# Kernel optimization log

Hardware: AMD Instinct MI355X
Metric: run time of the kernel (lower is better)

## Reference

```python
import jax, jax.numpy as jnp
import numpy as np

HIDDEN = 1024

def setup_inputs() -> dict:
    key = jax.random.key(0)
    k0, k1, k2, k3 = jax.random.split(key, 4)
    inputs = jax.random.normal(k0, (4, 2048, HIDDEN), dtype=jnp.float32)
    s = 1.0 / np.sqrt(HIDDEN)
    Wq = jax.random.normal(k1, (HIDDEN, HIDDEN), dtype=jnp.float32) * s
    Wk = jax.random.normal(k2, (HIDDEN, HIDDEN), dtype=jnp.float32) * s
    Wv = jax.random.normal(k3, (HIDDEN, HIDDEN), dtype=jnp.float32) * s
    return {"inputs": inputs, "Wq": Wq, "Wk": Wk, "Wv": Wv}

def reference(inputs, Wq, Wk, Wv):
    # nn.Linear with weight W applies x @ W.T; store Wq etc. as the torch weight.
    Q = jnp.einsum('bsd,ed->bse', inputs, Wq)  # [B,S,D]
    K = jnp.einsum('bsd,ed->bse', inputs, Wk)
    V = jnp.einsum('bsd,ed->bse', inputs, Wv)
    alpha = jnp.einsum('bqd,bkd->bqk', Q, K)   # no 1/sqrt(d) scaling, per source
    alpha = jax.nn.softmax(alpha, axis=2)
    return jnp.einsum('bqk,bkd->bqd', alpha, V)
```

## Files before the change

kernel.cpp:

```cpp
#include <hip/hip_runtime.h>
#include <math.h>


typedef unsigned short u16;
typedef signed char s8;
typedef __attribute__((ext_vector_type(8))) short bf16x8;
typedef __attribute__((ext_vector_type(4))) float f32x4;
typedef __attribute__((ext_vector_type(4))) int i32x4;

__device__ __forceinline__ u16 f2bf(float x) {
  unsigned u = __float_as_uint(x);
  unsigned r = (u + 0x7fffu + ((u >> 16) & 1u)) >> 16;
  return (u16)r;
}
__device__ __forceinline__ float bf2f(u16 h) {
  return __uint_as_float((unsigned)h << 16);
}
__device__ __forceinline__ int clamp127(int q) {
  return q < -127 ? -127 : (q > 127 ? 127 : q);
}

__device__ __forceinline__ void gload_lds16(const void* g, void* l) {
  __builtin_amdgcn_global_load_lds(
      (const __attribute__((address_space(1))) unsigned int*)(g),
      (__attribute__((address_space(3))) unsigned int*)(l), 16, 0, 0);
}

template <int N>
__device__ __forceinline__ void wait_vmcnt() {
  if constexpr (N == 0) asm volatile("s_waitcnt vmcnt(0)" ::: "memory");
  else if constexpr (N == 3) asm volatile("s_waitcnt vmcnt(3)" ::: "memory");
  else if constexpr (N == 4) asm volatile("s_waitcnt vmcnt(4)" ::: "memory");
  else if constexpr (N == 6) asm volatile("s_waitcnt vmcnt(6)" ::: "memory");
}

template <bool LO>
__global__ __launch_bounds__(256) void split_f32_kernel(
    const float* __restrict__ in, u16* __restrict__ hi, u16* __restrict__ lo,
    long long n) {
  long long i = ((long long)blockIdx.x * 256 + threadIdx.x) * 4;
  const long long step = (long long)gridDim.x * 256 * 4;
  for (; i < n; i += step) {
    float4 x = *(const float4*)(in + i);
    float xs[4] = {x.x, x.y, x.z, x.w};
    u16 hv[4], lv[4];
#pragma unroll
    for (int j = 0; j < 4; j++) {
      hv[j] = f2bf(xs[j]);
      if (LO) lv[j] = f2bf(xs[j] - bf2f(hv[j]));
    }
    ushort4 h;
    h.x = hv[0]; h.y = hv[1]; h.z = hv[2]; h.w = hv[3];
    *(ushort4*)(hi + i) = h;
    if (LO) {
      ushort4 l;
      l.x = lv[0]; l.y = lv[1]; l.z = lv[2]; l.w = lv[3];
      *(ushort4*)(lo + i) = l;
    }
  }
}

__global__ __launch_bounds__(256) void quantW3_kernel(
    const float* __restrict__ Wq, const float* __restrict__ Wk,
    const float* __restrict__ Wv, u16* __restrict__ Wch,
    u16* __restrict__ Wcl, u16* __restrict__ Wvh, long long n) {
  const int z = blockIdx.z;
  const float* src = (z == 0) ? Wq : ((z == 1) ? Wk : Wv);
  u16* hi = (z == 0) ? Wch : ((z == 1) ? (Wch + n) : Wvh);
  u16* lo = (z == 0) ? Wcl : ((z == 1) ? (Wcl + n) : nullptr);
  long long i = ((long long)blockIdx.x * 256 + threadIdx.x) * 4;
  const long long step = (long long)gridDim.x * 256 * 4;
  for (; i < n; i += step) {
    float4 x = *(const float4*)(src + i);
    float xs[4] = {x.x, x.y, x.z, x.w};
    u16 hv[4], lv[4];
#pragma unroll
    for (int j = 0; j < 4; j++) {
      hv[j] = f2bf(xs[j]);
      lv[j] = f2bf(xs[j] - bf2f(hv[j]));
    }
    ushort4 h;
    h.x = hv[0]; h.y = hv[1]; h.z = hv[2]; h.w = hv[3];
    *(ushort4*)(hi + i) = h;
    if (z < 2) {
      ushort4 l;
      l.x = lv[0]; l.y = lv[1]; l.z = lv[2]; l.w = lv[3];
      *(ushort4*)(lo + i) = l;
    }
  }
}

__global__ __launch_bounds__(512, 2) void gemmf(
    const u16* __restrict__ Xh, const u16* __restrict__ Xl,
    const u16* __restrict__ Wh, const u16* __restrict__ Wl,
    s8* __restrict__ Ca, s8* __restrict__ Cb) {
  constexpr int PL = 8192;
  __shared__ u16 lds[2 * 4 * PL];

  const int tid = threadIdx.x;
  const int ln = tid & 63;
  const int wid = tid >> 6;
  const int wm = wid >> 2;
  const int wn = wid & 3;
  const int m0 = blockIdx.y * 256;
  const int n0 = blockIdx.x * 256;

  f32x4 acc[8][4];
  const f32x4 zero = {0.f, 0.f, 0.f, 0.f};
#pragma unroll
  for (int i = 0; i < 8; i++)
#pragma unroll
    for (int j = 0; j < 4; j++) acc[i][j] = zero;

  auto stage = [&](int t) {
    u16* slot = lds + (t & 1) * 4 * PL;
    const int k0 = t << 5;
#pragma unroll
    for (int l = 0; l < 2; ++l) {
      const int c = tid + l * 512;
      const int row = ((c >> 6) << 4) + (c & 15);
      const int kk = ((c >> 4) & 3) * 8;
      gload_lds16(Xh + (size_t)(m0 + row) * 1024 + k0 + kk, slot + c * 8);
      gload_lds16(Xl + (size_t)(m0 + row) * 1024 + k0 + kk,
                  slot + PL + c * 8);
      gload_lds16(Wh + (size_t)(n0 + row) * 1024 + k0 + kk,
                  slot + 2 * PL + c * 8);
      gload_lds16(Wl + (size_t)(n0 + row) * 1024 + k0 + kk,
                  slot + 3 * PL + c * 8);
    }
  };

  stage(0);
  wait_vmcnt<0>();
  __builtin_amdgcn_s_barrier();
  __builtin_amdgcn_sched_barrier(0);

  for (int t = 0; t < 32; ++t) {
    if (t + 1 < 32) stage(t + 1);
    const u16* Ah = lds + (t & 1) * 4 * PL;
    const u16* Al = Ah + PL;
    const u16* Bh = Ah + 2 * PL;
    const u16* Bl = Ah + 3 * PL;
    const int fo = ln * 8;
    bf16x8 bh[4], bl[4];
#pragma unroll
    for (int j = 0; j < 4; ++j) {
      bh[j] = *(const bf16x8*)(Bh + (wn * 4 + j) * 512 + fo);
      bl[j] = *(const bf16x8*)(Bl + (wn * 4 + j) * 512 + fo);
    }
    __builtin_amdgcn_s_setprio(1);
#pragma unroll
    for (int mh = 0; mh < 2; ++mh) {
      bf16x8 ah[4], al[4];
#pragma unroll
      for (int i = 0; i < 4; ++i) {
        ah[i] = *(const bf16x8*)(Ah + (wm * 8 + mh * 4 + i) * 512 + fo);
        al[i] = *(const bf16x8*)(Al + (wm * 8 + mh * 4 + i) * 512 + fo);
      }
#pragma unroll
      for (int i = 0; i < 4; ++i)
#pragma unroll
        for (int j = 0; j < 4; ++j) {
          f32x4 v = acc[mh * 4 + i][j];
          v = __builtin_amdgcn_mfma_f32_16x16x32_bf16(ah[i], bh[j], v, 0, 0, 0);
          v = __builtin_amdgcn_mfma_f32_16x16x32_bf16(ah[i], bl[j], v, 0, 0, 0);
          v = __builtin_amdgcn_mfma_f32_16x16x32_bf16(al[i], bh[j], v, 0, 0, 0);
          acc[mh * 4 + i][j] = v;
        }
    }
    __builtin_amdgcn_s_setprio(0);
    if (t + 1 < 32) {
      wait_vmcnt<0>();
      __builtin_amdgcn_s_barrier();
      __builtin_amdgcn_sched_barrier(0);
    }
  }

  const int orow = (ln >> 4) * 4;
  const int ocol = ln & 15;
#pragma unroll
  for (int mi = 0; mi < 8; ++mi)
#pragma unroll
    for (int ni = 0; ni < 4; ++ni) {
      const int rbase = m0 + wm * 128 + mi * 16 + orow;
      const int cc = n0 + wn * 64 + ni * 16 + ocol;
#pragma unroll
      for (int i = 0; i < 4; ++i) {
        const float v = acc[mi][ni][i];
        const long long off = (long long)(rbase + i) * 2048 + cc;
        const int qa = clamp127(__float2int_rn(v * 16.f));
        const int qb = clamp127(__float2int_rn((v - qa * 0.0625f) * 2048.f));
        Ca[off] = (s8)qa;
        Cb[off] = (s8)qb;
      }
    }
}

__global__ __launch_bounds__(512, 2) void g2(
    const s8* __restrict__ Aa, const s8* __restrict__ Ab,
    const s8* __restrict__ Ba, const s8* __restrict__ Bb,
    u16* __restrict__ Ch, u16* __restrict__ Cl,
    int K, int lda, int ldb, int ldc,
    long long sA, long long sB, long long sC,
    float scaleA, float scaleC) {
  constexpr int APL = 128 * 64;
  constexpr int BPL = 256 * 64;
  constexpr int SLOT = 2 * APL + 2 * BPL;
  __shared__ s8 lds[3 * SLOT];

  const int tid = threadIdx.x;
  const int ln = tid & 63;
  const int wid = tid >> 6;
  const int wm = wid >> 2;
  const int wn = wid & 3;
  const int m0 = blockIdx.y * 128;
  const int n0 = blockIdx.x * 256;
  const int z = blockIdx.z;
  const long long za = (long long)z * sA;
  const long long zb = (long long)z * sB;

  const int NT = K >> 6;

  i32x4 accA[4][4], accC[4][4];
  const i32x4 izero = {0, 0, 0, 0};
#pragma unroll
  for (int i = 0; i < 4; i++)
#pragma unroll
    for (int j = 0; j < 4; j++) { accA[i][j] = izero; accC[i][j] = izero; }

  auto stage = [&](int t) {
    s8* slot = lds + (t % 3) * SLOT;
    const int k0 = t << 6;
    const s8* pAa = Aa + za + (size_t)m0 * lda + k0;
    const s8* pAb = Ab + za + (size_t)m0 * lda + k0;
    const s8* pBa = Ba + zb + (size_t)n0 * ldb + k0;
    const s8* pBb = Bb + zb + (size_t)n0 * ldb + k0;
    {
      const int c = tid;
      const int row = ((c >> 6) << 4) + (c & 15);
      const int kk = ((c >> 4) & 3) * 16;
      gload_lds16(pAa + (size_t)row * lda + kk, slot + c * 16);
      gload_lds16(pAb + (size_t)row * lda + kk, slot + APL + c * 16);
    }
#pragma unroll
    for (int l = 0; l < 2; ++l) {
      const int c = tid + l * 512;
      const int row = ((c >> 6) << 4) + (c & 15);
      const int kk = ((c >> 4) & 3) * 16;
      gload_lds16(pBa + (size_t)row * ldb + kk, slot + 2 * APL + c * 16);
      gload_lds16(pBb + (size_t)row * ldb + kk,
                  slot + 2 * APL + BPL + c * 16);
    }
  };

  stage(0);
  stage(1);
  wait_vmcnt<6>();
  __builtin_amdgcn_s_barrier();
  __builtin_amdgcn_sched_barrier(0);

  for (int t = 0; t < NT; ++t) {
    if (t + 2 < NT) stage(t + 2);
    const s8* Sa = lds + (t % 3) * SLOT;
    const s8* Sb = Sa + APL;
    const s8* Sba = Sa + 2 * APL;
    const s8* Sbb = Sba + BPL;
    const int fo = (ln >> 4) * 256 + (ln & 15) * 16;
    i32x4 aa[4], ab[4], ba[4], bb[4];
#pragma unroll
    for (int j = 0; j < 4; ++j) {
      ba[j] = *(const i32x4*)(Sba + (wn * 4 + j) * 1024 + fo);
      bb[j] = *(const i32x4*)(Sbb + (wn * 4 + j) * 1024 + fo);
    }
#pragma unroll
    for (int i = 0; i < 4; ++i) {
      aa[i] = *(const i32x4*)(Sa + (wm * 4 + i) * 1024 + fo);
      ab[i] = *(const i32x4*)(Sb + (wm * 4 + i) * 1024 + fo);
    }
    __builtin_amdgcn_s_setprio(1);
#pragma unroll
    for (int i = 0; i < 4; ++i)
#pragma unroll
      for (int j = 0; j < 4; ++j) {
        accA[i][j] = __builtin_amdgcn_mfma_i32_16x16x64_i8(
            aa[i], ba[j], accA[i][j], 0, 0, 0);
        accC[i][j] = __builtin_amdgcn_mfma_i32_16x16x64_i8(
            aa[i], bb[j], accC[i][j], 0, 0, 0);
        accC[i][j] = __builtin_amdgcn_mfma_i32_16x16x64_i8(
            ab[i], ba[j], accC[i][j], 0, 0, 0);
      }
    __builtin_amdgcn_s_setprio(0);
    if (t + 1 < NT) {
      if (t + 2 < NT) wait_vmcnt<6>();
      else            wait_vmcnt<0>();
      __builtin_amdgcn_s_barrier();
      __builtin_amdgcn_sched_barrier(0);
    }
  }

  const int orow = (ln >> 4) * 4;
  const int ocol = ln & 15;
#pragma unroll
  for (int mi = 0; mi < 4; ++mi)
#pragma unroll
    for (int ni = 0; ni < 4; ++ni) {
      const int rbase = m0 + wm * 64 + mi * 16 + orow;
      const int cc = n0 + wn * 64 + ni * 16 + ocol;
#pragma unroll
      for (int i = 0; i < 4; ++i) {
        const float v = (float)accA[mi][ni][i] * scaleA +
                        (float)accC[mi][ni][i] * scaleC;
        const long long off =
            (long long)(rbase + i) * ldc + cc + (long long)z * sC;
        const u16 h = f2bf(v);
        Ch[off] = h;
        Cl[off] = f2bf(v - bf2f(h));
      }
    }
}

template <int STORE>
__global__ __launch_bounds__(512, 2) void gemmc64(
    const u16* __restrict__ A0, const u16* __restrict__ B0,
    float* __restrict__ Cf, u16* __restrict__ Ch,
    int K, int lda, int ldb, int ldc,
    long long sA, long long sB, long long sC) {
  constexpr int ASZ = 128 * 64;
  constexpr int BSZ = 256 * 64;
  constexpr int SLOT = ASZ + BSZ;
  __shared__ u16 lds[3 * SLOT];

  const int tid = threadIdx.x;
  const int ln = tid & 63;
  const int wid = tid >> 6;
  const int wm = wid >> 2;
  const int wn = wid & 3;
  const int m0 = blockIdx.y * 128;
  const int n0 = blockIdx.x * 256;
  const int z = blockIdx.z;
  const long long za = (long long)z * sA;
  const long long zb = (long long)z * sB;

  const int NT = K >> 6;

  f32x4 acc[4][4];
  const f32x4 zero = {0.f, 0.f, 0.f, 0.f};
#pragma unroll
  for (int i = 0; i < 4; i++)
#pragma unroll
    for (int j = 0; j < 4; j++) acc[i][j] = zero;

  auto stage = [&](int t) {
    u16* slot = lds + (t % 3) * SLOT;
    const int k0 = t << 6;
    const u16* Ab = A0 + za + (size_t)m0 * lda + k0;
    const u16* Bb = B0 + zb + (size_t)n0 * ldb + k0;
#pragma unroll
    for (int l = 0; l < 2; ++l) {
      const int c = tid + l * 512;
      const int row = c >> 3;
      const int jg = (c & 7) ^ (row & 7);
      gload_lds16(Ab + (size_t)row * lda + jg * 8, slot + c * 8);
    }
#pragma unroll
    for (int l = 0; l < 4; ++l) {
      const int c = tid + l * 512;
      const int row = c >> 3;
      const int jg = (c & 7) ^ (row & 7);
      gload_lds16(Bb + (size_t)row * ldb + jg * 8, slot + ASZ + c * 8);
    }
  };

  stage(0);
  stage(1);
  wait_vmcnt<6>();
  __builtin_amdgcn_s_barrier();
  __builtin_amdgcn_sched_barrier(0);

  const int r15 = ln & 15;
  const int jk = ln >> 4;
  const int sw0 = ((jk ^ (r15 & 7)) * 8);
  const int sw1 = (((4 + jk) ^ (r15 & 7)) * 8);

  for (int t = 0; t < NT; ++t) {
    if (t + 2 < NT) stage(t + 2);
    const u16* Abuf = lds + (t % 3) * SLOT;
    const u16* Bbuf = Abuf + ASZ;
    bf16x8 a0[4], a1[4], b0[4], b1[4];
#pragma unroll
    for (int j = 0; j < 4; ++j) {
      const int rb = ((wn * 4 + j) * 16 + r15) * 64;
      b0[j] = *(const bf16x8*)(Bbuf + rb + sw0);
      b1[j] = *(const bf16x8*)(Bbuf + rb + sw1);
    }
#pragma unroll
    for (int i = 0; i < 4; ++i) {
      const int ra = ((wm * 4 + i) * 16 + r15) * 64;
      a0[i] = *(const bf16x8*)(Abuf + ra + sw0);
      a1[i] = *(const bf16x8*)(Abuf + ra + sw1);
    }
    __builtin_amdgcn_s_setprio(1);
#pragma unroll
    for (int i = 0; i < 4; ++i)
#pragma unroll
      for (int j = 0; j < 4; ++j) {
        acc[i][j] = __builtin_amdgcn_mfma_f32_16x16x32_bf16(
            a0[i], b0[j], acc[i][j], 0, 0, 0);
        acc[i][j] = __builtin_amdgcn_mfma_f32_16x16x32_bf16(
            a1[i], b1[j], acc[i][j], 0, 0, 0);
      }
    __builtin_amdgcn_s_setprio(0);
    if (t + 1 < NT) {
      if (t + 2 < NT) wait_vmcnt<6>();
      else            wait_vmcnt<0>();
      __builtin_amdgcn_s_barrier();
      __builtin_amdgcn_sched_barrier(0);
    }
  }

  const int orow = (ln >> 4) * 4;
  const int ocol = ln & 15;
#pragma unroll
  for (int mi = 0; mi < 4; ++mi)
#pragma unroll
    for (int ni = 0; ni < 4; ++ni) {
      const int rbase = m0 + wm * 64 + mi * 16 + orow;
      const int cc = n0 + wn * 64 + ni * 16 + ocol;
#pragma unroll
      for (int i = 0; i < 4; ++i) {
        const float v = acc[mi][ni][i];
        const long long off =
            (long long)(rbase + i) * ldc + cc + (long long)z * sC;
        if (STORE == 0) Cf[off] = v;
        else            Ch[off] = f2bf(v);
      }
    }
}

template <int NSEG, int STORE, int M_REP>
__global__ __launch_bounds__(512, 2) void gemmc(
    const u16* __restrict__ A0, const u16* __restrict__ A1,
    const u16* __restrict__ A2, const u16* __restrict__ B0,
    const u16* __restrict__ B1, const u16* __restrict__ B2,
    float* __restrict__ Cf, u16* __restrict__ Ch, u16* __restrict__ Cl,
    int Kseg, int lda, int ldb, int ldc,
    long long sA, long long sB, long long sC) {
  constexpr int BM = 32 * M_REP;
  constexpr int ASZ = BM * 32;
  constexpr int BSZ = 8192;
  constexpr int SLOT = ASZ + BSZ;
  constexpr int LA = M_REP / 4;
  constexpr int L = LA + 2;
  __shared__ u16 lds[3 * SLOT];

  const int tid = threadIdx.x;
  const int ln = tid & 63;
  const int wid = tid >> 6;
  const int wm = wid >> 2;
  const int wn = wid & 3;
  const int m0 = blockIdx.y * BM;
  const int n0 = blockIdx.x * 256;
  const int z = blockIdx.z;
  const long long za = (long long)z * sA;
  const long long zb = (long long)z * sB;

  const int NT = NSEG * (Kseg >> 5);

  f32x4 acc[M_REP][4];
  const f32x4 zero = {0.f, 0.f, 0.f, 0.f};
#pragma unroll
  for (int i = 0; i < M_REP; i++)
#pragma unroll
    for (int j = 0; j < 4; j++) acc[i][j] = zero;

  auto baseA = [&](int t) -> const u16* {
    int kk = t << 5;
    const u16* p = A0;
    if (NSEG >= 2 && kk >= Kseg) { kk -= Kseg; p = A1; }
    if (NSEG >= 3 && kk >= Kseg) { kk -= Kseg; p = A2; }
    return p + za + (size_t)m0 * lda + kk;
  };
  auto baseB = [&](int t) -> const u16* {
    int kk = t << 5;
    const u16* p = B0;
    if (NSEG >= 2 && kk >= Kseg) { kk -= Kseg; p = B1; }
    if (NSEG >= 3 && kk >= Kseg) { kk -= Kseg; p = B2; }
    return p + zb + (size_t)n0 * ldb + kk;
  };
  auto stage = [&](int t) {
    u16* slot = lds + (t % 3) * SLOT;
    const u16* Ab = baseA(t);
    const u16* Bb = baseB(t);
#pragma unroll
    for (int l = 0; l < LA; ++l) {
      const int c = tid + l * 512;
      const int row = ((c >> 6) << 4) + (c & 15);
      const int kk = ((c >> 4) & 3) * 8;
      gload_lds16(Ab + (size_t)row * lda + kk, slot + c * 8);
    }
#pragma unroll
    for (int l = 0; l < 2; ++l) {
      const int c = tid + l * 512;
      const int row = ((c >> 6) << 4) + (c & 15);
      const int kk = ((c >> 4) & 3) * 8;
      gload_lds16(Bb + (size_t)row * ldb + kk, slot + ASZ + c * 8);
    }
  };

  stage(0);
  stage(1);
  wait_vmcnt<L>();
  __builtin_amdgcn_s_barrier();
  __builtin_amdgcn_sched_barrier(0);

  for (int t = 0; t < NT; ++t) {
    if (t + 2 < NT) stage(t + 2);
    const u16* Abuf = lds + (t % 3) * SLOT;
    const u16* Bbuf = Abuf + ASZ;
    const int fo = ln * 8;
    bf16x8 a[M_REP], b[4];
#pragma unroll
    for (int j = 0; j < 4; ++j)
      b[j] = *(const bf16x8*)(Bbuf + (wn * 4 + j) * 512 + fo);
#pragma unroll
    for (int i = 0; i < M_REP; ++i)
      a[i] = *(const bf16x8*)(Abuf + (wm * M_REP + i) * 512 + fo);
    __builtin_amdgcn_s_setprio(1);
#pragma unroll
    for (int i = 0; i < M_REP; ++i)
#pragma unroll
      for (int j = 0; j < 4; ++j)
        acc[i][j] = __builtin_amdgcn_mfma_f32_16x16x32_bf16(
            a[i], b[j], acc[i][j], 0, 0, 0);
    __builtin_amdgcn_s_setprio(0);
    if (t + 1 < NT) {
      if (t + 2 < NT) wait_vmcnt<L>();
      else            wait_vmcnt<0>();
      __builtin_amdgcn_s_barrier();
      __builtin_amdgcn_sched_barrier(0);
    }
  }

  const int orow = (ln >> 4) * 4;
  const int ocol = ln & 15;
#pragma unroll
  for (int mi = 0; mi < M_REP; ++mi)
#pragma unroll
    for (int ni = 0; ni < 4; ++ni) {
      const int rbase = m0 + wm * (M_REP * 16) + mi * 16 + orow;
      const int cc = n0 + wn * 64 + ni * 16 + ocol;
#pragma unroll
      for (int i = 0; i < 4; ++i) {
        const float v = acc[mi][ni][i];
        const long long off =
            (long long)(rbase + i) * ldc + cc + (long long)z * sC;
        if (STORE == 0) {
          Cf[off] = v;
        } else if (STORE == 1) {
          const u16 h = f2bf(v);
          Ch[off] = h;
          Cl[off] = f2bf(v - bf2f(h));
        } else {
          Ch[off] = f2bf(v);
        }
      }
    }
}

__device__ __forceinline__ float blk_max(float v, float* red) {
  const int wv = threadIdx.x >> 6, lnn = threadIdx.x & 63;
#pragma unroll
  for (int off = 32; off; off >>= 1) v = fmaxf(v, __shfl_xor(v, off));
  if (lnn == 0) red[wv] = v;
  __syncthreads();
  return fmaxf(fmaxf(red[0], red[1]), fmaxf(red[2], red[3]));
}
__device__ __forceinline__ float blk_sum(float v, float* red) {
  const int wv = threadIdx.x >> 6, lnn = threadIdx.x & 63;
#pragma unroll
  for (int off = 32; off; off >>= 1) v += __shfl_xor(v, off);
  if (lnn == 0) red[wv] = v;
  __syncthreads();
  return red[0] + red[1] + red[2] + red[3];
}

__global__ __launch_bounds__(256) void softmax_inplace(float* __restrict__ L) {
  float* p = L + (size_t)blockIdx.x * 2048;
  const int t = threadIdx.x;
  __shared__ float redm[4];
  __shared__ float reds[4];
  float4 x0 = *(const float4*)(p + t * 4);
  float4 x1 = *(const float4*)(p + 1024 + t * 4);
  float m = fmaxf(fmaxf(fmaxf(x0.x, x0.y), fmaxf(x0.z, x0.w)),
                  fmaxf(fmaxf(x1.x, x1.y), fmaxf(x1.z, x1.w)));
  m = blk_max(m, redm);
  float e[8];
  e[0] = __expf(x0.x - m); e[1] = __expf(x0.y - m);
  e[2] = __expf(x0.z - m); e[3] = __expf(x0.w - m);
  e[4] = __expf(x1.x - m); e[5] = __expf(x1.y - m);
  e[6] = __expf(x1.z - m); e[7] = __expf(x1.w - m);
  float s = e[0] + e[1] + e[2] + e[3] + e[4] + e[5] + e[6] + e[7];
  s = blk_sum(s, reds);
  const float inv = 1.f / s;
  u16* q = (u16*)p;
  ushort4 o0, o1;
  o0.x = f2bf(e[0] * inv); o0.y = f2bf(e[1] * inv);
  o0.z = f2bf(e[2] * inv); o0.w = f2bf(e[3] * inv);
  o1.x = f2bf(e[4] * inv); o1.y = f2bf(e[5] * inv);
  o1.z = f2bf(e[6] * inv); o1.w = f2bf(e[7] * inv);
  *(ushort4*)(q + t * 4) = o0;
  *(ushort4*)(q + 1024 + t * 4) = o1;
}

__global__ __launch_bounds__(256) void softmax_split(
    u16* __restrict__ Lh, const u16* __restrict__ Ll) {
  u16* ph = Lh + (size_t)blockIdx.x * 2048;
  const u16* pl = Ll + (size_t)blockIdx.x * 2048;
  const int t = threadIdx.x;
  __shared__ float redm[4];
  __shared__ float reds[4];
  ushort4 h0 = *(const ushort4*)(ph + t * 4);
  ushort4 h1 = *(const ushort4*)(ph + 1024 + t * 4);
  ushort4 l0 = *(const ushort4*)(pl + t * 4);
  ushort4 l1 = *(const ushort4*)(pl + 1024 + t * 4);
  float x[8];
  x[0] = bf2f(h0.x) + bf2f(l0.x); x[1] = bf2f(h0.y) + bf2f(l0.y);
  x[2] = bf2f(h0.z) + bf2f(l0.z); x[3] = bf2f(h0.w) + bf2f(l0.w);
  x[4] = bf2f(h1.x) + bf2f(l1.x); x[5] = bf2f(h1.y) + bf2f(l1.y);
  x[6] = bf2f(h1.z) + bf2f(l1.z); x[7] = bf2f(h1.w) + bf2f(l1.w);
  float m = fmaxf(fmaxf(fmaxf(x[0], x[1]), fmaxf(x[2], x[3])),
                  fmaxf(fmaxf(x[4], x[5]), fmaxf(x[6], x[7])));
  m = blk_max(m, redm);
  float e[8];
#pragma unroll
  for (int j = 0; j < 8; ++j) e[j] = __expf(x[j] - m);
  float s = e[0] + e[1] + e[2] + e[3] + e[4] + e[5] + e[6] + e[7];
  s = blk_sum(s, reds);
  const float inv = 1.f / s;
  ushort4 o0, o1;
  o0.x = f2bf(e[0] * inv); o0.y = f2bf(e[1] * inv);
  o0.z = f2bf(e[2] * inv); o0.w = f2bf(e[3] * inv);
  o1.x = f2bf(e[4] * inv); o1.y = f2bf(e[5] * inv);
  o1.z = f2bf(e[6] * inv); o1.w = f2bf(e[7] * inv);
  *(ushort4*)(ph + t * 4) = o0;
  *(ushort4*)(ph + 1024 + t * 4) = o1;
}

extern "C" void kernel_launch(void* const* d_in, const int* in_sizes, int n_in,
                              void* d_out, int out_size, void* d_ws, size_t ws_size,
                              hipStream_t stream) {
  constexpr int Bn = 4, S = 2048, D = 1024;
  constexpr long long TOK = (long long)Bn * S;
  constexpr long long DD = (long long)D * D;
  const float* X = (const float*)d_in[0];
  const float* Wq = (const float*)d_in[1];
  const float* Wk = (const float*)d_in[2];
  const float* Wv = (const float*)d_in[3];
  float* out = (float*)d_out;
  const dim3 blk(256);
  const dim3 gblk(512);

  char* w = (char*)d_ws;
  auto au16 = [&](long long n) { u16* p = (u16*)w; w += n * 2; return p; };
  auto as8 = [&](long long n) { s8* p = (s8*)w; w += n; return p; };

  if (ws_size >= (size_t)127926272ULL) {
    u16* Xh = au16(TOK * D);
    u16* Xl = au16(TOK * D);
    u16* Wch = au16(2 * DD);
    u16* Wcl = au16(2 * DD);
    u16* Wvh = au16(DD);
    s8* QKa = as8(TOK * 2 * D);
    s8* QKb = as8(TOK * 2 * D);
    u16* VT = au16((long long)D * TOK);
    u16* Ll = au16(TOK * S);
    u16* Lh = (u16*)d_ws;

    split_f32_kernel<true><<<2048, blk, 0, stream>>>(X, Xh, Xl, TOK * D);
    quantW3_kernel<<<dim3(256, 1, 3), blk, 0, stream>>>(
        Wq, Wk, Wv, Wch, Wcl, Wvh, DD);

    gemmf<<<dim3(8, 32, 1), gblk, 0, stream>>>(
        Xh, Xl, Wch, Wcl, QKa, QKb);
    gemmc64<2><<<dim3(32, 8, 1), gblk, 0, stream>>>(
        Wvh, Xh, nullptr, VT, D, D, D, (int)TOK, 0, 0, 0);

    g2<<<dim3(8, 16, 4), gblk, 0, stream>>>(
        QKa, QKb, QKa + D, QKb + D, Lh, Ll,
        D, 2 * D, 2 * D, S,
        (long long)S * 2 * D, (long long)S * 2 * D, (long long)S * S,
        3.90625e-3f, 3.0517578125e-5f);
    softmax_split<<<dim3(4 * S), blk, 0, stream>>>(Lh, Ll);
    gemmc64<0><<<dim3(4, 16, 4), gblk, 0, stream>>>(
        Lh, VT, out, nullptr, S, S, (int)TOK, D,
        (long long)S * S, (long long)S, (long long)S * D);
  } else {
    u16* Xh = au16(TOK * D);
    u16* Xl = au16(TOK * D);
    u16* Wch = au16(2 * DD);
    u16* Wcl = au16(2 * DD);
    u16* Wvh = au16(DD);
    u16* QKhb = au16((long long)S * 2 * D);
    u16* QKlb = au16((long long)S * 2 * D);
    u16* VTb = au16((long long)D * S);
    float* Lb = (float*)w;

    split_f32_kernel<true><<<2048, blk, 0, stream>>>(X, Xh, Xl, TOK * D);
    split_f32_kernel<true><<<512, blk, 0, stream>>>(Wq, Wch, Wcl, DD);
    split_f32_kernel<true><<<512, blk, 0, stream>>>(Wk, Wch + DD, Wcl + DD, DD);
    split_f32_kernel<false><<<512, blk, 0, stream>>>(Wv, Wvh, nullptr, DD);

    for (int b = 0; b < Bn; ++b) {
      const long long xo = (long long)b * S * D;
      gemmc<3, 1, 8><<<dim3(8, 8, 1), gblk, 0, stream>>>(
          Xh + xo, Xh + xo, Xl + xo, Wch, Wcl, Wch, nullptr, QKhb, QKlb,
          D, D, D, 2 * D, 0, 0, 0);
      gemmc<1, 2, 4><<<dim3(8, 8, 1), gblk, 0, stream>>>(
          Wvh, nullptr, nullptr, Xh + xo, nullptr, nullptr, nullptr, VTb,
          nullptr, D, D, D, S, 0, 0, 0);
      gemmc<3, 0, 4><<<dim3(8, 16, 1), gblk, 0, stream>>>(
          QKhb, QKhb, QKlb, QKhb + D, QKlb + D, QKhb + D,
          Lb, nullptr, nullptr, D, 2 * D, 2 * D, S, 0, 0, 0);
      softmax_inplace<<<dim3(S), blk, 0, stream>>>(Lb);
      gemmc<1, 0, 4><<<dim3(4, 16, 1), gblk, 0, stream>>>(
          (const u16*)Lb, nullptr, nullptr, VTb, nullptr, nullptr,
          out + xo, nullptr, nullptr, S, 2 * S, S, D, 0, 0, 0);
    }
  }
}
```

Baseline: 247.8 us.

## Restructure int8 QK^T GEMM to 128x128 tiles with swizzled double-buffered LDS

Measured after the change: 243.8 us. Within noise of the previous version (-1.6%).

```diff
diff --git a/kernel.cpp b/kernel.cpp
--- a/kernel.cpp
+++ b/kernel.cpp
@@ -29,7 +29,6 @@
 template <int N>
 __device__ __forceinline__ void wait_vmcnt() {
   if constexpr (N == 0) asm volatile("s_waitcnt vmcnt(0)" ::: "memory");
-  else if constexpr (N == 3) asm volatile("s_waitcnt vmcnt(3)" ::: "memory");
   else if constexpr (N == 4) asm volatile("s_waitcnt vmcnt(4)" ::: "memory");
   else if constexpr (N == 6) asm volatile("s_waitcnt vmcnt(6)" ::: "memory");
 }
@@ -196,17 +195,15 @@
     }
 }
 
-__global__ __launch_bounds__(512, 2) void g2(
+__global__ __launch_bounds__(512, 2) void g2p(
     const s8* __restrict__ Aa, const s8* __restrict__ Ab,
     const s8* __restrict__ Ba, const s8* __restrict__ Bb,
     u16* __restrict__ Ch, u16* __restrict__ Cl,
     int K, int lda, int ldb, int ldc,
     long long sA, long long sB, long long sC,
     float scaleA, float scaleC) {
-  constexpr int APL = 128 * 64;
-  constexpr int BPL = 256 * 64;
-  constexpr int SLOT = 2 * APL + 2 * BPL;
-  __shared__ s8 lds[3 * SLOT];
+  constexpr int PL = 128 * 128;
+  __shared__ s8 lds[2 * 4 * PL];
 
   const int tid = threadIdx.x;
   const int ln = tid & 63;
@@ -214,85 +211,83 @@
   const int wm = wid >> 2;
   const int wn = wid & 3;
   const int m0 = blockIdx.y * 128;
-  const int n0 = blockIdx.x * 256;
+  const int n0 = blockIdx.x * 128;
   const int z = blockIdx.z;
   const long long za = (long long)z * sA;
   const long long zb = (long long)z * sB;
 
-  const int NT = K >> 6;
-
-  i32x4 accA[4][4], accC[4][4];
+  const int NT = K >> 7;
+
+  i32x4 accA[4][2], accC[4][2];
   const i32x4 izero = {0, 0, 0, 0};
 #pragma unroll
   for (int i = 0; i < 4; i++)
 #pragma unroll
-    for (int j = 0; j < 4; j++) { accA[i][j] = izero; accC[i][j] = izero; }
+    for (int j = 0; j < 2; j++) { accA[i][j] = izero; accC[i][j] = izero; }
 
   auto stage = [&](int t) {
-    s8* slot = lds + (t % 3) * SLOT;
-    const int k0 = t << 6;
+    s8* slot = lds + (t & 1) * 4 * PL;
+    const int k0 = t << 7;
     const s8* pAa = Aa + za + (size_t)m0 * lda + k0;
     const s8* pAb = Ab + za + (size_t)m0 * lda + k0;
     const s8* pBa = Ba + zb + (size_t)n0 * ldb + k0;
     const s8* pBb = Bb + zb + (size_t)n0 * ldb + k0;
-    {
-      const int c = tid;
-      const int row = ((c >> 6) << 4) + (c & 15);
-      const int kk = ((c >> 4) & 3) * 16;
-      gload_lds16(pAa + (size_t)row * lda + kk, slot + c * 16);
-      gload_lds16(pAb + (size_t)row * lda + kk, slot + APL + c * 16);
-    }
 #pragma unroll
     for (int l = 0; l < 2; ++l) {
       const int c = tid + l * 512;
-      const int row = ((c >> 6) << 4) + (c & 15);
-      const int kk = ((c >> 4) & 3) * 16;
-      gload_lds16(pBa + (size_t)row * ldb + kk, slot + 2 * APL + c * 16);
-      gload_lds16(pBb + (size_t)row * ldb + kk,
-                  slot + 2 * APL + BPL + c * 16);
+      const int row = c >> 3;
+      const int j8 = (c & 7) ^ (row & 7);
+      gload_lds16(pAa + (size_t)row * lda + j8 * 16, slot + c * 16);
+      gload_lds16(pAb + (size_t)row * lda + j8 * 16, slot + PL + c * 16);
+      gload_lds16(pBa + (size_t)row * ldb + j8 * 16, slot + 2 * PL + c * 16);
+      gload_lds16(pBb + (size_t)row * ldb + j8 * 16, slot + 3 * PL + c * 16);
     }
   };
 
   stage(0);
-  stage(1);
-  wait_vmcnt<6>();
+  wait_vmcnt<0>();
   __builtin_amdgcn_s_barrier();
   __builtin_amdgcn_sched_barrier(0);
 
+  const int r15 = ln & 15;
+  const int jk = ln >> 4;
+
   for (int t = 0; t < NT; ++t) {
-    if (t + 2 < NT) stage(t + 2);
-    const s8* Sa = lds + (t % 3) * SLOT;
-    const s8* Sb = Sa + APL;
-    const s8* Sba = Sa + 2 * APL;
-    const s8* Sbb = Sba + BPL;
-    const int fo = (ln >> 4) * 256 + (ln & 15) * 16;
-    i32x4 aa[4], ab[4], ba[4], bb[4];
-#pragma unroll
-    for (int j = 0; j < 4; ++j) {
-      ba[j] = *(const i32x4*)(Sba + (wn * 4 + j) * 1024 + fo);
-      bb[j] = *(const i32x4*)(Sbb + (wn * 4 + j) * 1024 + fo);
-    }
-#pragma unroll
-    for (int i = 0; i < 4; ++i) {
-      aa[i] = *(const i32x4*)(Sa + (wm * 4 + i) * 1024 + fo);
-      ab[i] = *(const i32x4*)(Sb + (wm * 4 + i) * 1024 + fo);
-    }
-    __builtin_amdgcn_s_setprio(1);
-#pragma unroll
-    for (int i = 0; i < 4; ++i)
-#pragma unroll
-      for (int j = 0; j < 4; ++j) {
-        accA[i][j] = __builtin_amdgcn_mfma_i32_16x16x64_i8(
-            aa[i], ba[j], accA[i][j], 0, 0, 0);
-        accC[i][j] = __builtin_amdgcn_mfma_i32_16x16x64_i8(
-            aa[i], bb[j], accC[i][j], 0, 0, 0);
-        accC[i][j] = __builtin_amdgcn_mfma_i32_16x16x64_i8(
-            ab[i], ba[j], accC[i][j], 0, 0, 0);
+    if (t + 1 < NT) stage(t + 1);
+    const s8* base = lds + (t & 1) * 4 * PL;
+#pragma unroll
+    for (int ks = 0; ks < 2; ++ks) {
+      i32x4 aa[4], ab[4], ba[2], bb[2];
+#pragma unroll
+      for (int j = 0; j < 2; ++j) {
+        const int row = wn * 32 + j * 16 + r15;
+        const int off = row * 128 + (((ks * 4 + jk) ^ (row & 7)) * 16);
+        ba[j] = *(const i32x4*)(base + 2 * PL + off);
+        bb[j] = *(const i32x4*)(base + 3 * PL + off);
       }
-    __builtin_amdgcn_s_setprio(0);
+#pragma unroll
+      for (int i = 0; i < 4; ++i) {
+        const int row = wm * 64 + i * 16 + r15;
+        const int off = row * 128 + (((ks * 4 + jk) ^ (row & 7)) * 16);
+        aa[i] = *(const i32x4*)(base + off);
+        ab[i] = *(const i32x4*)(base + PL + off);
+      }
+      __builtin_amdgcn_s_setprio(1);
+#pragma unroll
+      for (int i = 0; i < 4; ++i)
+#pragma unroll
+        for (int j = 0; j < 2; ++j) {
+          accA[i][j] = __builtin_amdgcn_mfma_i32_16x16x64_i8(
+              aa[i], ba[j], accA[i][j], 0, 0, 0);
+          accC[i][j] = __builtin_amdgcn_mfma_i32_16x16x64_i8(
+              aa[i], bb[j], accC[i][j], 0, 0, 0);
+          accC[i][j] = __builtin_amdgcn_mfma_i32_16x16x64_i8(
+              ab[i], ba[j], accC[i][j], 0, 0, 0);
+        }
+      __builtin_amdgcn_s_setprio(0);
+    }
     if (t + 1 < NT) {
-      if (t + 2 < NT) wait_vmcnt<6>();
-      else            wait_vmcnt<0>();
+      wait_vmcnt<0>();
       __builtin_amdgcn_s_barrier();
       __builtin_amdgcn_sched_barrier(0);
     }
@@ -303,9 +298,9 @@
 #pragma unroll
   for (int mi = 0; mi < 4; ++mi)
 #pragma unroll
-    for (int ni = 0; ni < 4; ++ni) {
+    for (int ni = 0; ni < 2; ++ni) {
       const int rbase = m0 + wm * 64 + mi * 16 + orow;
-      const int cc = n0 + wn * 64 + ni * 16 + ocol;
+      const int cc = n0 + wn * 32 + ni * 16 + ocol;
 #pragma unroll
       for (int i = 0; i < 4; ++i) {
         const float v = (float)accA[mi][ni][i] * scaleA +
@@ -685,7 +680,7 @@
     gemmc64<2><<<dim3(32, 8, 1), gblk, 0, stream>>>(
         Wvh, Xh, nullptr, VT, D, D, D, (int)TOK, 0, 0, 0);
 
-    g2<<<dim3(8, 16, 4), gblk, 0, stream>>>(
+    g2p<<<dim3(16, 16, 4), gblk, 0, stream>>>(
         QKa, QKb, QKa + D, QKb + D, Lh, Ll,
         D, 2 * D, 2 * D, S,
         (long long)S * 2 * D, (long long)S * 2 * D, (long long)S * S,
```
